# Kernel tuning notes

Measured on AMD Instinct MI355X. Metric: run time of the kernel, lower is better.

The kernel has to match this reference:

```python
import jax, jax.numpy as jnp
from jax import lax
import numpy as np

B, C, H, W = 32, 256, 56, 56
K = 3
EPS = 1e-5


def setup_inputs() -> dict:
    key = jax.random.key(0)
    k1, k2, k3, k4 = jax.random.split(key, 4)
    x = jax.random.normal(k1, (B, C, H, W), dtype=jnp.float32)
    # xavier_normal init for conv weight [C_out, C_in, K, K]
    fan_in = C * K * K
    fan_out = C * K * K
    std = float(np.sqrt(2.0 / (fan_in + fan_out)))
    w = jax.random.normal(k2, (C, C, K, K), dtype=jnp.float32) * std
    gamma = jnp.ones((C,), dtype=jnp.float32)
    beta = jnp.zeros((C,), dtype=jnp.float32)
    return {"x": x, "w": w, "gamma": gamma, "beta": beta}


def reference(x, w, gamma, beta):
    # --- Binarize (bi_act_method=0, bi_w_scale=1) ---
    bx = jnp.sign(x)                                   # activation sign
    wc = jnp.clip(w, -1.0, 1.0)                        # fp_weight.data.clamp_(-1,1)
    mean_val = jnp.mean(jnp.abs(wc))
    bw = jnp.sign(wc) * mean_val                       # sign(w) * mean(|w|)
    # --- float conv2d, stride 1, padding 1 ---
    out = lax.conv_general_dilated(
        bx, bw, window_strides=(1, 1), padding=[(1, 1), (1, 1)],
        dimension_numbers=("NCHW", "OIHW", "NCHW"))
    # --- identity shortcut (stride=1, C_in==C_out) ---
    out = out + x
    # --- BatchNorm2d (training-mode batch stats, affine) ---
    mean = jnp.mean(out, axis=(0, 2, 3), keepdims=True)
    var = jnp.var(out, axis=(0, 2, 3), keepdims=True)
    out = (out - mean) * lax.rsqrt(var + EPS)
    out = out * gamma[None, :, None, None] + beta[None, :, None, None]
    # --- ReLU ---
    return jax.nn.relu(out)
```

## Files before the change

### kernel.cpp

```cpp
#include <hip/hip_runtime.h>
#include <cstdint>

#define Bn   32
#define Cn   256
#define Hn   56
#define Wn   56
#define HWn  (Hn*Wn)
#define NTOT (Bn*Cn*HWn)
#define WELEMS (Cn*Cn*9)
#define EPSv 1e-5f

#define PR   58
#define PPB  (PR*PR)

#define F_WABS  0
#define F_SUM   64
#define F_SQ    320
#define STATS_BYTES 4096
#define CLS_OFF_BYTES 4096
#define WB_OFF_BYTES  16384
#define XB_OFF_BYTES  98304
#define XB_BYTES (Bn*PPB*8*4)

__global__ void pack_w_kernel(const float* __restrict__ w,
                              float* __restrict__ wsf,
                              uint32_t* __restrict__ wb) {
    int u = blockIdx.x * 256 + threadIdx.x;
    float sabs = 0.0f;
    {
        int co = u / 72;
        int r  = u % 72;
        int t  = r >> 3;
        int wd = r & 7;
        uint32_t bits = 0;
        const float* wp = w + (size_t)co * 2304 + (size_t)(wd * 32) * 9 + t;
        #pragma unroll
        for (int j = 0; j < 32; j++) {
            float wv = wp[(size_t)j * 9];
            sabs += fminf(fabsf(wv), 1.0f);
            bits |= (__float_as_uint(wv) >> 31) << j;
        }
        wb[u] = bits;
    }
    #pragma unroll
    for (int off = 32; off; off >>= 1) sabs += __shfl_down(sabs, off);
    __shared__ float sh[4];
    if ((threadIdx.x & 63) == 0) sh[threadIdx.x >> 6] = sabs;
    __syncthreads();
    if (threadIdx.x == 0)
        atomicAdd(&wsf[F_WABS], sh[0] + sh[1] + sh[2] + sh[3]);
}

__global__ void wtable_kernel(const uint32_t* __restrict__ wb,
                              int* __restrict__ clst) {
    int co = threadIdx.x;
    int wp[9];
    #pragma unroll
    for (int t = 0; t < 9; t++) {
        int s = 0;
        #pragma unroll
        for (int wd = 0; wd < 8; wd++) s += __popc(wb[(co * 9 + t) * 8 + wd]);
        wp[t] = 256 - 2 * s;
    }
    int T = wp[0] + wp[1] + wp[2];
    int Bm = wp[6] + wp[7] + wp[8];
    int L = wp[0] + wp[3] + wp[6];
    int R = wp[2] + wp[5] + wp[8];
    int* o = clst + co * 9;
    o[0] = 0;
    o[1] = L;
    o[2] = R;
    o[3] = T;
    o[4] = T + L - wp[0];
    o[5] = T + R - wp[2];
    o[6] = Bm;
    o[7] = Bm + L - wp[6];
    o[8] = Bm + R - wp[8];
}

__global__ void pack_x_kernel(const float* __restrict__ x,
                              uint32_t* __restrict__ xb) {
    int v = blockIdx.x * 256 + threadIdx.x;
    int b = v / HWn;
    int p = v - b * HWn;
    int y = p / Wn;
    int xq = p - y * Wn;
    const float* xp = x + (size_t)b * Cn * HWn + p;
    uint32_t r[8];
    #pragma unroll
    for (int wd = 0; wd < 8; wd++) {
        uint32_t bits = 0;
        #pragma unroll
        for (int j = 0; j < 32; j++) {
            bits |= (__float_as_uint(xp[(size_t)(wd * 32 + j) * HWn]) >> 31) << j;
        }
        r[wd] = bits;
    }
    size_t dst = (size_t)b * PPB + (size_t)(y + 1) * PR + (xq + 1);
    uint4* d = (uint4*)xb + dst * 2;
    d[0] = make_uint4(r[0], r[1], r[2], r[3]);
    d[1] = make_uint4(r[4], r[5], r[6], r[7]);
}

__global__ __launch_bounds__(256) void conv_kernel(
    const uint32_t* __restrict__ xb, const uint32_t* __restrict__ wb,
    const int* __restrict__ clst,
    const float* __restrict__ x, const float* __restrict__ wsf,
    float* __restrict__ out) {
    int v = blockIdx.x * 256 + threadIdx.x;
    int b = v / HWn;
    int p = v - b * HWn;
    int y = p / Wn;
    int xq = p - y * Wn;
    int co0 = blockIdx.y * 8;

    const float mean_val = wsf[F_WABS] * (1.0f / (float)WELEMS);

    const uint4* base = (const uint4*)xb + ((size_t)b * PPB + (size_t)y * PR + xq) * 2;

    int acc[8] = {0, 0, 0, 0, 0, 0, 0, 0};
    #pragma unroll
    for (int dh = 0; dh < 3; dh++) {
        uint32_t nw[24];
        const uint4* rp = base + dh * (PR * 2);
        #pragma unroll
        for (int q = 0; q < 6; q++) {
            uint4 t = rp[q];
            nw[q * 4 + 0] = t.x; nw[q * 4 + 1] = t.y;
            nw[q * 4 + 2] = t.z; nw[q * 4 + 3] = t.w;
        }
        #pragma unroll
        for (int dw = 0; dw < 3; dw++) {
            #pragma unroll
            for (int cs = 0; cs < 8; cs++) {
                const uint32_t* wp = wb + ((size_t)(co0 + cs) * 9 + (dh * 3 + dw)) * 8;
                int pc = acc[cs];
                #pragma unroll
                for (int wd = 0; wd < 8; wd++)
                    pc += __popc(nw[dw * 8 + wd] ^ wp[wd]);
                acc[cs] = pc;
            }
        }
    }

    int yp = (y == 0) ? 1 : ((y == 55) ? 2 : 0);
    int xp = (xq == 0) ? 1 : ((xq == 55) ? 2 : 0);
    int cls = yp * 3 + xp;

    #pragma unroll
    for (int cs = 0; cs < 8; cs++) {
        int corr = clst[(co0 + cs) * 9 + cls];
        size_t idx = ((size_t)b * Cn + (co0 + cs)) * HWn + p;
        float dot = (float)(2304 - 2 * acc[cs] - corr);
        out[idx] = fmaf(mean_val, dot, x[idx]);
    }
}

__global__ void stats_kernel(const float* __restrict__ out,
                             float* __restrict__ wsf) {
    int plane = blockIdx.x;
    const float4* p = (const float4*)(out + (size_t)plane * HWn);
    float s = 0.0f, q = 0.0f;
    for (int i = threadIdx.x; i < HWn / 4; i += 256) {
        float4 v = p[i];
        s += v.x + v.y + v.z + v.w;
        q += v.x * v.x + v.y * v.y + v.z * v.z + v.w * v.w;
    }
    #pragma unroll
    for (int off = 32; off; off >>= 1) {
        s += __shfl_down(s, off);
        q += __shfl_down(q, off);
    }
    __shared__ float ss[4], sq[4];
    if ((threadIdx.x & 63) == 0) { ss[threadIdx.x >> 6] = s; sq[threadIdx.x >> 6] = q; }
    __syncthreads();
    if (threadIdx.x == 0) {
        int c = plane & 255;
        atomicAdd(&wsf[F_SUM + c], ss[0] + ss[1] + ss[2] + ss[3]);
        atomicAdd(&wsf[F_SQ  + c], sq[0] + sq[1] + sq[2] + sq[3]);
    }
}

__global__ void epilogue_kernel(float* __restrict__ out,
                                const float* __restrict__ wsf,
                                const float* __restrict__ g,
                                const float* __restrict__ bt) {
    int plane = blockIdx.x;
    int c = plane & 255;
    const float n = (float)(Bn * HWn);
    float mean = wsf[F_SUM + c] / n;
    float var  = wsf[F_SQ + c] / n - mean * mean;
    float sc = g[c] * rsqrtf(var + EPSv);
    float sh = bt[c] - mean * sc;
    float4* o4 = (float4*)(out + (size_t)plane * HWn);
    for (int i = threadIdx.x; i < HWn / 4; i += 256) {
        float4 v = o4[i];
        v.x = fmaxf(fmaf(v.x, sc, sh), 0.0f);
        v.y = fmaxf(fmaf(v.y, sc, sh), 0.0f);
        v.z = fmaxf(fmaf(v.z, sc, sh), 0.0f);
        v.w = fmaxf(fmaf(v.w, sc, sh), 0.0f);
        o4[i] = v;
    }
}

extern "C" void kernel_launch(void* const* d_in, const int* in_sizes, int n_in,
                              void* d_out, int out_size, void* d_ws, size_t ws_size,
                              hipStream_t stream) {
    const float* x     = (const float*)d_in[0];
    const float* w     = (const float*)d_in[1];
    const float* gamma = (const float*)d_in[2];
    const float* beta  = (const float*)d_in[3];
    float* out = (float*)d_out;

    float*    wsf  = (float*)d_ws;
    int*      clst = (int*)((char*)d_ws + CLS_OFF_BYTES);
    uint32_t* wb   = (uint32_t*)((char*)d_ws + WB_OFF_BYTES);
    uint32_t* xb   = (uint32_t*)((char*)d_ws + XB_OFF_BYTES);

    hipMemsetAsync(d_ws, 0, STATS_BYTES, stream);
    hipMemsetAsync(xb, 0, XB_BYTES, stream);
    pack_w_kernel<<<dim3(72), dim3(256), 0, stream>>>(w, wsf, wb);
    wtable_kernel<<<dim3(1), dim3(256), 0, stream>>>(wb, clst);
    pack_x_kernel<<<dim3(392), dim3(256), 0, stream>>>(x, xb);
    conv_kernel<<<dim3(392, 32), dim3(256), 0, stream>>>(xb, wb, clst, x, wsf, out);
    stats_kernel<<<dim3(Bn * Cn), dim3(256), 0, stream>>>(out, wsf);
    epilogue_kernel<<<dim3(Bn * Cn), dim3(256), 0, stream>>>(out, wsf, gamma, beta);
}
```

Before: 353.3 us.

## Replace XNOR-popcount conv with int8 MFMA implicit GEMM and fused stats

Binarized activations and weights are now stored as ±1 int8 values, and zero padding is kept as literal zeros so the border-correction table is no longer needed. The conv becomes an implicit GEMM on the matrix cores using mfma_i32_16x16x64_i8, with each block covering 256 output channels by 128 pixels. The BatchNorm sum and sum-of-squares are accumulated in the conv epilogue through shuffles and atomics, which removes the separate stats pass over the output. The cost is an 8x larger packed activation buffer to memset and write, plus atomic contention on the per-channel stats.

```diff
diff --git a/kernel.cpp b/kernel.cpp
--- a/kernel.cpp
+++ b/kernel.cpp
@@ -6,41 +6,44 @@
 #define Hn   56
 #define Wn   56
 #define HWn  (Hn*Wn)
-#define NTOT (Bn*Cn*HWn)
+#define NPIX (Bn*HWn)
 #define WELEMS (Cn*Cn*9)
 #define EPSv 1e-5f
 
 #define PR   58
-#define PPB  (PR*PR)
+#define PPLANE (PR*PR)
 
 #define F_WABS  0
 #define F_SUM   64
 #define F_SQ    320
 #define STATS_BYTES 4096
-#define CLS_OFF_BYTES 4096
-#define WB_OFF_BYTES  16384
-#define XB_OFF_BYTES  98304
-#define XB_BYTES (Bn*PPB*8*4)
-
-__global__ void pack_w_kernel(const float* __restrict__ w,
-                              float* __restrict__ wsf,
-                              uint32_t* __restrict__ wb) {
+#define WPK_OFF  4096
+#define WPK_BYTES WELEMS
+#define ACT_OFF  (WPK_OFF + WPK_BYTES)
+#define ACT_BYTES (Bn*PPLANE*Cn)
+
+typedef int v4i __attribute__((ext_vector_type(4)));
+
+__global__ void pack_w_i8(const float* __restrict__ w,
+                          float* __restrict__ wsf,
+                          int8_t* __restrict__ wpk) {
     int u = blockIdx.x * 256 + threadIdx.x;
+    int co = u / 9;
+    int t  = u - co * 9;
+    const float* wp = w + (size_t)co * 2304 + t;
+    uint32_t* dst = (uint32_t*)(wpk + ((size_t)co * 9 + t) * 256);
     float sabs = 0.0f;
-    {
-        int co = u / 72;
-        int r  = u % 72;
-        int t  = r >> 3;
-        int wd = r & 7;
-        uint32_t bits = 0;
-        const float* wp = w + (size_t)co * 2304 + (size_t)(wd * 32) * 9 + t;
-        #pragma unroll
-        for (int j = 0; j < 32; j++) {
-            float wv = wp[(size_t)j * 9];
+    #pragma unroll
+    for (int cw = 0; cw < 64; cw++) {
+        uint32_t r = 0;
+        #pragma unroll
+        for (int j = 0; j < 4; j++) {
+            float wv = wp[(size_t)(cw * 4 + j) * 9];
             sabs += fminf(fabsf(wv), 1.0f);
-            bits |= (__float_as_uint(wv) >> 31) << j;
-        }
-        wb[u] = bits;
+            uint32_t byte = (__float_as_uint(wv) >> 31) ? 0xFFu : 0x01u;
+            r |= byte << (j * 8);
+        }
+        dst[cw] = r;
     }
     #pragma unroll
     for (int off = 32; off; off >>= 1) sabs += __shfl_down(sabs, off);
@@ -51,133 +54,116 @@
         atomicAdd(&wsf[F_WABS], sh[0] + sh[1] + sh[2] + sh[3]);
 }
 
-__global__ void wtable_kernel(const uint32_t* __restrict__ wb,
-                              int* __restrict__ clst) {
-    int co = threadIdx.x;
-    int wp[9];
-    #pragma unroll
-    for (int t = 0; t < 9; t++) {
-        int s = 0;
-        #pragma unroll
-        for (int wd = 0; wd < 8; wd++) s += __popc(wb[(co * 9 + t) * 8 + wd]);
-        wp[t] = 256 - 2 * s;
-    }
-    int T = wp[0] + wp[1] + wp[2];
-    int Bm = wp[6] + wp[7] + wp[8];
-    int L = wp[0] + wp[3] + wp[6];
-    int R = wp[2] + wp[5] + wp[8];
-    int* o = clst + co * 9;
-    o[0] = 0;
-    o[1] = L;
-    o[2] = R;
-    o[3] = T;
-    o[4] = T + L - wp[0];
-    o[5] = T + R - wp[2];
-    o[6] = Bm;
-    o[7] = Bm + L - wp[6];
-    o[8] = Bm + R - wp[8];
-}
-
-__global__ void pack_x_kernel(const float* __restrict__ x,
-                              uint32_t* __restrict__ xb) {
+__global__ void pack_x_i8(const float* __restrict__ x,
+                          int8_t* __restrict__ act) {
     int v = blockIdx.x * 256 + threadIdx.x;
     int b = v / HWn;
     int p = v - b * HWn;
     int y = p / Wn;
-    int xq = p - y * Wn;
+    int xx = p - y * Wn;
     const float* xp = x + (size_t)b * Cn * HWn + p;
-    uint32_t r[8];
-    #pragma unroll
-    for (int wd = 0; wd < 8; wd++) {
-        uint32_t bits = 0;
-        #pragma unroll
-        for (int j = 0; j < 32; j++) {
-            bits |= (__float_as_uint(xp[(size_t)(wd * 32 + j) * HWn]) >> 31) << j;
-        }
-        r[wd] = bits;
-    }
-    size_t dst = (size_t)b * PPB + (size_t)(y + 1) * PR + (xq + 1);
-    uint4* d = (uint4*)xb + dst * 2;
-    d[0] = make_uint4(r[0], r[1], r[2], r[3]);
-    d[1] = make_uint4(r[4], r[5], r[6], r[7]);
-}
-
-__global__ __launch_bounds__(256) void conv_kernel(
-    const uint32_t* __restrict__ xb, const uint32_t* __restrict__ wb,
-    const int* __restrict__ clst,
-    const float* __restrict__ x, const float* __restrict__ wsf,
+    uint32_t* dst = (uint32_t*)(act + ((size_t)(b * PR + (y + 1)) * PR + (xx + 1)) * 256);
+    #pragma unroll
+    for (int cw = 0; cw < 64; cw++) {
+        uint32_t r = 0;
+        #pragma unroll
+        for (int j = 0; j < 4; j++) {
+            uint32_t sgn = __float_as_uint(xp[(size_t)(cw * 4 + j) * HWn]) >> 31;
+            r |= (sgn ? 0xFFu : 0x01u) << (j * 8);
+        }
+        dst[cw] = r;
+    }
+}
+
+__global__ __launch_bounds__(256, 2) void conv_mfma(
+    const int8_t* __restrict__ act, const int8_t* __restrict__ wpk,
+    const float* __restrict__ x, float* __restrict__ wsf,
     float* __restrict__ out) {
-    int v = blockIdx.x * 256 + threadIdx.x;
-    int b = v / HWn;
-    int p = v - b * HWn;
-    int y = p / Wn;
-    int xq = p - y * Wn;
-    int co0 = blockIdx.y * 8;
-
-    const float mean_val = wsf[F_WABS] * (1.0f / (float)WELEMS);
-
-    const uint4* base = (const uint4*)xb + ((size_t)b * PPB + (size_t)y * PR + xq) * 2;
-
-    int acc[8] = {0, 0, 0, 0, 0, 0, 0, 0};
-    #pragma unroll
-    for (int dh = 0; dh < 3; dh++) {
-        uint32_t nw[24];
-        const uint4* rp = base + dh * (PR * 2);
-        #pragma unroll
-        for (int q = 0; q < 6; q++) {
-            uint4 t = rp[q];
-            nw[q * 4 + 0] = t.x; nw[q * 4 + 1] = t.y;
-            nw[q * 4 + 2] = t.z; nw[q * 4 + 3] = t.w;
-        }
-        #pragma unroll
-        for (int dw = 0; dw < 3; dw++) {
-            #pragma unroll
-            for (int cs = 0; cs < 8; cs++) {
-                const uint32_t* wp = wb + ((size_t)(co0 + cs) * 9 + (dh * 3 + dw)) * 8;
-                int pc = acc[cs];
+    const int lane = threadIdx.x & 63;
+    const int wid  = threadIdx.x >> 6;
+    const int co_w = wid * 64;
+    const int p0   = blockIdx.x * 128;
+    const int l15  = lane & 15;
+    const int l4   = lane >> 4;
+
+    int bofs[8];
+    int obase[8];
+    #pragma unroll
+    for (int ni = 0; ni < 8; ni++) {
+        int n = p0 + ni * 16 + l15;
+        int b = n / HWn;
+        int p = n - b * HWn;
+        int y = p / Wn;
+        int xx = p - y * Wn;
+        bofs[ni] = ((b * PR + (y + 1)) * PR + (xx + 1)) * 256 + l4 * 16;
+        obase[ni] = b * (Cn * HWn) + p;
+    }
+    int aofs[4];
+    #pragma unroll
+    for (int mi = 0; mi < 4; mi++)
+        aofs[mi] = (co_w + mi * 16 + l15) * 2304 + l4 * 16;
+
+    v4i acc[4][8] = {};
+
+    for (int t = 0; t < 9; t++) {
+        const int dh = t / 3 - 1;
+        const int dw = t % 3 - 1;
+        const int toff = (dh * PR + dw) * 256;
+        #pragma unroll
+        for (int s = 0; s < 4; s++) {
+            const int koff = t * 256 + s * 64;
+            v4i af[4], bf[8];
+            #pragma unroll
+            for (int mi = 0; mi < 4; mi++)
+                af[mi] = *(const v4i*)(wpk + aofs[mi] + koff);
+            #pragma unroll
+            for (int ni = 0; ni < 8; ni++)
+                bf[ni] = *(const v4i*)(act + bofs[ni] + toff + s * 64);
+            #pragma unroll
+            for (int mi = 0; mi < 4; mi++) {
                 #pragma unroll
-                for (int wd = 0; wd < 8; wd++)
-                    pc += __popc(nw[dw * 8 + wd] ^ wp[wd]);
-                acc[cs] = pc;
-            }
-        }
-    }
-
-    int yp = (y == 0) ? 1 : ((y == 55) ? 2 : 0);
-    int xp = (xq == 0) ? 1 : ((xq == 55) ? 2 : 0);
-    int cls = yp * 3 + xp;
-
-    #pragma unroll
-    for (int cs = 0; cs < 8; cs++) {
-        int corr = clst[(co0 + cs) * 9 + cls];
-        size_t idx = ((size_t)b * Cn + (co0 + cs)) * HWn + p;
-        float dot = (float)(2304 - 2 * acc[cs] - corr);
-        out[idx] = fmaf(mean_val, dot, x[idx]);
-    }
-}
-
-__global__ void stats_kernel(const float* __restrict__ out,
-                             float* __restrict__ wsf) {
-    int plane = blockIdx.x;
-    const float4* p = (const float4*)(out + (size_t)plane * HWn);
-    float s = 0.0f, q = 0.0f;
-    for (int i = threadIdx.x; i < HWn / 4; i += 256) {
-        float4 v = p[i];
-        s += v.x + v.y + v.z + v.w;
-        q += v.x * v.x + v.y * v.y + v.z * v.z + v.w * v.w;
-    }
-    #pragma unroll
-    for (int off = 32; off; off >>= 1) {
-        s += __shfl_down(s, off);
-        q += __shfl_down(q, off);
-    }
-    __shared__ float ss[4], sq[4];
-    if ((threadIdx.x & 63) == 0) { ss[threadIdx.x >> 6] = s; sq[threadIdx.x >> 6] = q; }
-    __syncthreads();
-    if (threadIdx.x == 0) {
-        int c = plane & 255;
-        atomicAdd(&wsf[F_SUM + c], ss[0] + ss[1] + ss[2] + ss[3]);
-        atomicAdd(&wsf[F_SQ  + c], sq[0] + sq[1] + sq[2] + sq[3]);
+                for (int ni = 0; ni < 8; ni++)
+                    acc[mi][ni] = __builtin_amdgcn_mfma_i32_16x16x64_i8(
+                        af[mi], bf[ni], acc[mi][ni], 0, 0, 0);
+            }
+        }
+    }
+
+    const float mv = wsf[F_WABS] * (1.0f / (float)WELEMS);
+
+    float ssum[4][4] = {}, ssq[4][4] = {};
+    #pragma unroll
+    for (int mi = 0; mi < 4; mi++) {
+        #pragma unroll
+        for (int ni = 0; ni < 8; ni++) {
+            v4i a = acc[mi][ni];
+            #pragma unroll
+            for (int q = 0; q < 4; q++) {
+                int co = co_w + mi * 16 + l4 * 4 + q;
+                size_t idx = (size_t)obase[ni] + (size_t)co * HWn;
+                float val = fmaf(mv, (float)a[q], x[idx]);
+                out[idx] = val;
+                ssum[mi][q] += val;
+                ssq[mi][q]  += val * val;
+            }
+        }
+    }
+    #pragma unroll
+    for (int mi = 0; mi < 4; mi++) {
+        #pragma unroll
+        for (int q = 0; q < 4; q++) {
+            float s = ssum[mi][q], sq = ssq[mi][q];
+            #pragma unroll
+            for (int off = 1; off < 16; off <<= 1) {
+                s  += __shfl_xor(s, off);
+                sq += __shfl_xor(sq, off);
+            }
+            if (l15 == 0) {
+                int co = co_w + mi * 16 + l4 * 4 + q;
+                atomicAdd(&wsf[F_SUM + co], s);
+                atomicAdd(&wsf[F_SQ  + co], sq);
+            }
+        }
     }
 }
 
@@ -212,17 +198,14 @@
     const float* beta  = (const float*)d_in[3];
     float* out = (float*)d_out;
 
-    float*    wsf  = (float*)d_ws;
-    int*      clst = (int*)((char*)d_ws + CLS_OFF_BYTES);
-    uint32_t* wb   = (uint32_t*)((char*)d_ws + WB_OFF_BYTES);
-    uint32_t* xb   = (uint32_t*)((char*)d_ws + XB_OFF_BYTES);
+    float*  wsf = (float*)d_ws;
+    int8_t* wpk = (int8_t*)d_ws + WPK_OFF;
+    int8_t* act = (int8_t*)d_ws + ACT_OFF;
 
     hipMemsetAsync(d_ws, 0, STATS_BYTES, stream);
-    hipMemsetAsync(xb, 0, XB_BYTES, stream);
-    pack_w_kernel<<<dim3(72), dim3(256), 0, stream>>>(w, wsf, wb);
-    wtable_kernel<<<dim3(1), dim3(256), 0, stream>>>(wb, clst);
-    pack_x_kernel<<<dim3(392), dim3(256), 0, stream>>>(x, xb);
-    conv_kernel<<<dim3(392, 32), dim3(256), 0, stream>>>(xb, wb, clst, x, wsf, out);
-    stats_kernel<<<dim3(Bn * Cn), dim3(256), 0, stream>>>(out, wsf);
+    hipMemsetAsync(act, 0, ACT_BYTES, stream);
+    pack_w_i8<<<dim3(9),   dim3(256), 0, stream>>>(w, wsf, wpk);
+    pack_x_i8<<<dim3(392), dim3(256), 0, stream>>>(x, act);
+    conv_mfma<<<dim3(784), dim3(256), 0, stream>>>(act, wpk, x, wsf, out);
     epilogue_kernel<<<dim3(Bn * Cn), dim3(256), 0, stream>>>(out, wsf, gamma, beta);
 }
```

Result: slower. 509.7 us (+44.3%).
